# Kernel optimization log

Measured on AMD Instinct MI355X. Metric: run time of the kernel, lower is better.

## Reference

```python
import jax, jax.numpy as jnp
import numpy as np

N_NODES = 20000
N_EDGES = 640000
HIDDEN = 128


def setup_inputs() -> dict:
    key = jax.random.key(0)
    k1, k2, k3, k4 = jax.random.split(key, 4)
    scale = 1.0 / np.sqrt(HIDDEN)
    features = jax.random.normal(k1, (N_NODES, HIDDEN), dtype=jnp.float32)
    edge_index = jax.random.randint(k2, (2, N_EDGES), 0, N_NODES, dtype=jnp.int64)
    W_l = jax.random.normal(k3, (HIDDEN, HIDDEN), dtype=jnp.float32) * scale
    b_l = jnp.zeros((HIDDEN,), dtype=jnp.float32)
    W_r = jax.random.normal(k4, (HIDDEN, HIDDEN), dtype=jnp.float32) * scale
    return {"features": features, "edge_index": edge_index, "W_l": W_l, "b_l": b_l, "W_r": W_r}


def reference(features, edge_index, W_l, b_l, W_r):
    # PyG SAGEConv with mean aggregation:
    #   out_i = lin_l(mean_{j : (j->i) in E} x_j) + lin_r(x_i)
    # edge_index[0] = source nodes, edge_index[1] = target nodes.
    n = features.shape[0]
    src = edge_index[0]
    dst = edge_index[1]
    msg = features[src]  # [E, d] gather
    summed = jax.ops.segment_sum(msg, dst, num_segments=n)  # [N, d] scatter-add
    cnt = jax.ops.segment_sum(jnp.ones(src.shape[0], dtype=features.dtype), dst, num_segments=n)
    agg = summed / jnp.maximum(cnt, 1.0)[:, None]  # mean; isolated nodes -> 0
    return agg @ W_l.T + b_l + features @ W_r.T
```

## Files before the change

kernel.cpp:

```cpp
#include <hip/hip_runtime.h>

#define N_NODES 20000
#define N_EDGES 640000
#define HIDDEN  128
#define CAP     96
#define DEG_PAD 16
#define GEMM_BLOCKS 313
#define FILL_BLOCKS 2500

typedef unsigned short bf16_t;
typedef __attribute__((ext_vector_type(8))) short short8;
typedef __attribute__((ext_vector_type(4))) float floatx4;

__device__ __forceinline__ bf16_t f2bf(float f) {
    union { float f; unsigned int i; } v; v.f = f;
    unsigned int x = v.i + 0x7FFFu + ((v.i >> 16) & 1u);
    return (bf16_t)(x >> 16);
}
__device__ __forceinline__ float bflo(unsigned u) {
    union { unsigned i; float f; } v; v.i = u << 16; return v.f;
}
__device__ __forceinline__ float bfhi(unsigned u) {
    union { unsigned i; float f; } v; v.i = u & 0xFFFF0000u; return v.f;
}

__global__ void prep_kernel(const float* __restrict__ feat,
                            const float* __restrict__ Wl,
                            const float* __restrict__ Wr,
                            bf16_t* __restrict__ feat_bf,
                            bf16_t* __restrict__ Bp,
                            int* __restrict__ deg) {
    int t = blockIdx.x * 256 + threadIdx.x;
    float4 v = ((const float4*)feat)[t];
    ushort4 o = { f2bf(v.x), f2bf(v.y), f2bf(v.z), f2bf(v.w) };
    ((ushort4*)feat_bf)[t] = o;
    if (t < (N_NODES * DEG_PAD) / 4) {
        int4 zz = {0, 0, 0, 0};
        ((int4*)deg)[t] = zz;
    }
    if (t < 2 * HIDDEN * HIDDEN) {
        int j    = t & 7;
        int lane = (t >> 3) & 63;
        int nt   = (t >> 9) & 15;
        int kt   = t >> 13;
        int n = nt * 16 + (lane & 15);
        int k = kt * 32 + (lane >> 4) * 8 + j;
        float w = (n < HIDDEN) ? Wl[n * HIDDEN + k] : Wr[(n - HIDDEN) * HIDDEN + k];
        Bp[t] = f2bf(w);
    }
}

__global__ __launch_bounds__(256) void gemm_fill_kernel(
        const bf16_t* __restrict__ feat_bf,
        const bf16_t* __restrict__ Bp,
        const float* __restrict__ bl,
        const int* __restrict__ eidx,
        bf16_t* __restrict__ Y,
        float* __restrict__ Z,
        int* __restrict__ deg,
        int* __restrict__ bucket) {
    if (blockIdx.x < GEMM_BLOCKS) {
        int wid = blockIdx.x * 4 + (threadIdx.x >> 6);
        if (wid >= N_NODES / 16) return;
        int lane = threadIdx.x & 63;
        int m    = lane & 15;
        int quad = lane >> 4;
        int row0 = wid * 16;

        floatx4 acc[16];
        floatx4 zf = {0.f, 0.f, 0.f, 0.f};
#pragma unroll
        for (int nt = 0; nt < 16; ++nt) acc[nt] = zf;

        const short8* bp = (const short8*)Bp;
#pragma unroll
        for (int kt = 0; kt < 4; ++kt) {
            short8 afrag = *(const short8*)(feat_bf + (size_t)(row0 + m) * HIDDEN
                                            + kt * 32 + quad * 8);
#pragma unroll
            for (int nt = 0; nt < 16; ++nt) {
                short8 bfrag = bp[(kt * 16 + nt) * 64 + lane];
                acc[nt] = __builtin_amdgcn_mfma_f32_16x16x32_bf16(afrag, bfrag, acc[nt], 0, 0, 0);
            }
        }
        int col = lane & 15;
#pragma unroll
        for (int nt = 0; nt < 8; ++nt) {
#pragma unroll
            for (int r = 0; r < 4; ++r) {
                int row = row0 + quad * 4 + r;
                Y[(size_t)row * HIDDEN + nt * 16 + col] = f2bf(acc[nt][r]);
            }
        }
#pragma unroll
        for (int nt = 8; nt < 16; ++nt) {
            float b = bl[(nt - 8) * 16 + col];
#pragma unroll
            for (int r = 0; r < 4; ++r) {
                int row = row0 + quad * 4 + r;
                Z[(size_t)row * HIDDEN + (nt - 8) * 16 + col] = acc[nt][r] + b;
            }
        }
    } else {
        int e = (blockIdx.x - GEMM_BLOCKS) * 256 + threadIdx.x;
        if (e >= N_EDGES) return;
        int src = eidx[e];
        int dst = eidx[N_EDGES + e];
        int pos = atomicAdd(&deg[dst * DEG_PAD], 1);
        if (pos < CAP) bucket[dst * CAP + pos] = src;
    }
}

__global__ __launch_bounds__(256) void gather_final_kernel(
        const bf16_t* __restrict__ Y,
        const float* __restrict__ Z,
        const int* __restrict__ deg,
        const int* __restrict__ bucket,
        float* __restrict__ out) {
    int wid  = (blockIdx.x * 256 + threadIdx.x) >> 6;
    int lane = threadIdx.x & 63;
    if (wid >= N_NODES) return;
    int d_true = deg[wid * DEG_PAD];
    int d = min(d_true, CAP);
    const int* row = bucket + wid * CAP;
    const unsigned* y = (const unsigned*)Y;
    float ax0=0,ay0=0, ax1=0,ay1=0, ax2=0,ay2=0, ax3=0,ay3=0;
    int i = 0;
    for (; i + 4 <= d; i += 4) {
        int4 s = *(const int4*)(row + i);
        unsigned u0 = y[s.x * 64 + lane];
        unsigned u1 = y[s.y * 64 + lane];
        unsigned u2 = y[s.z * 64 + lane];
        unsigned u3 = y[s.w * 64 + lane];
        ax0 += bflo(u0); ay0 += bfhi(u0);
        ax1 += bflo(u1); ay1 += bfhi(u1);
        ax2 += bflo(u2); ay2 += bfhi(u2);
        ax3 += bflo(u3); ay3 += bfhi(u3);
    }
    for (; i < d; ++i) {
        unsigned u = y[row[i] * 64 + lane];
        ax0 += bflo(u); ay0 += bfhi(u);
    }
    float inv = 1.0f / fmaxf((float)d_true, 1.0f);
    float2 z = ((const float2*)Z)[wid * 64 + lane];
    float2 r;
    r.x = (ax0 + ax1 + ax2 + ax3) * inv + z.x;
    r.y = (ay0 + ay1 + ay2 + ay3) * inv + z.y;
    ((float2*)out)[wid * 64 + lane] = r;
}

extern "C" void kernel_launch(void* const* d_in, const int* in_sizes, int n_in,
                              void* d_out, int out_size, void* d_ws, size_t ws_size,
                              hipStream_t stream) {
    const float* feat = (const float*)d_in[0];
    const int*   eidx = (const int*)d_in[1];
    const float* Wl   = (const float*)d_in[2];
    const float* bl   = (const float*)d_in[3];
    const float* Wr   = (const float*)d_in[4];
    float* out = (float*)d_out;

    int*    deg     = (int*)d_ws;
    int*    bucket  = deg + N_NODES * DEG_PAD;
    bf16_t* Bp      = (bf16_t*)(bucket + N_NODES * CAP);
    bf16_t* feat_bf = Bp + 2 * HIDDEN * HIDDEN;
    bf16_t* Y       = feat_bf + (size_t)N_NODES * HIDDEN;
    float*  Z       = (float*)(Y + (size_t)N_NODES * HIDDEN);

    prep_kernel<<<2500, 256, 0, stream>>>(feat, Wl, Wr, feat_bf, Bp, deg);
    gemm_fill_kernel<<<GEMM_BLOCKS + FILL_BLOCKS, 256, 0, stream>>>(
        feat_bf, Bp, bl, eidx, Y, Z, deg, bucket);
    gather_final_kernel<<<(N_NODES * 64 + 255) / 256, 256, 0, stream>>>(
        Y, Z, deg, bucket, out);
}
```

Baseline: 142.1 us.

## Move edge bucketing into prep kernel, use 16-bit bucket indices, unroll gather by 8

The edge bucket fill now runs in the bf16 conversion kernel (each thread converts features and inserts one edge), and the degree array is zeroed with a memset. The GEMM gets its own kernel. Bucket entries shrink to 16-bit source indices, which halves bucket traffic, and the gather loop loads eight neighbours per iteration. This adds a memset launch and relies on node indices fitting in 16 bits, which holds since N_NODES is 20000.

```diff
diff --git a/kernel.cpp b/kernel.cpp
--- a/kernel.cpp
+++ b/kernel.cpp
@@ -5,11 +5,10 @@
 #define HIDDEN  128
 #define CAP     96
 #define DEG_PAD 16
-#define GEMM_BLOCKS 313
-#define FILL_BLOCKS 2500
 
 typedef unsigned short bf16_t;
 typedef __attribute__((ext_vector_type(8))) short short8;
+typedef __attribute__((ext_vector_type(8))) unsigned short ushort8_t;
 typedef __attribute__((ext_vector_type(4))) float floatx4;
 
 __device__ __forceinline__ bf16_t f2bf(float f) {
@@ -24,20 +23,23 @@
     union { unsigned i; float f; } v; v.i = u & 0xFFFF0000u; return v.f;
 }
 
-__global__ void prep_kernel(const float* __restrict__ feat,
-                            const float* __restrict__ Wl,
-                            const float* __restrict__ Wr,
-                            bf16_t* __restrict__ feat_bf,
-                            bf16_t* __restrict__ Bp,
-                            int* __restrict__ deg) {
+__global__ __launch_bounds__(256) void prep_fill_kernel(
+        const float* __restrict__ feat,
+        const float* __restrict__ Wl,
+        const float* __restrict__ Wr,
+        const int* __restrict__ eidx,
+        bf16_t* __restrict__ feat_bf,
+        bf16_t* __restrict__ Bp,
+        int* __restrict__ deg,
+        unsigned short* __restrict__ bucket) {
     int t = blockIdx.x * 256 + threadIdx.x;
     float4 v = ((const float4*)feat)[t];
     ushort4 o = { f2bf(v.x), f2bf(v.y), f2bf(v.z), f2bf(v.w) };
     ((ushort4*)feat_bf)[t] = o;
-    if (t < (N_NODES * DEG_PAD) / 4) {
-        int4 zz = {0, 0, 0, 0};
-        ((int4*)deg)[t] = zz;
-    }
+    int src = eidx[t];
+    int dst = eidx[N_EDGES + t];
+    int pos = atomicAdd(&deg[dst * DEG_PAD], 1);
+    if (pos < CAP) bucket[dst * CAP + pos] = (unsigned short)src;
     if (t < 2 * HIDDEN * HIDDEN) {
         int j    = t & 7;
         int lane = (t >> 3) & 63;
@@ -50,64 +52,52 @@
     }
 }
 
-__global__ __launch_bounds__(256) void gemm_fill_kernel(
+__global__ __launch_bounds__(256) void gemm_kernel(
         const bf16_t* __restrict__ feat_bf,
         const bf16_t* __restrict__ Bp,
         const float* __restrict__ bl,
-        const int* __restrict__ eidx,
         bf16_t* __restrict__ Y,
-        float* __restrict__ Z,
-        int* __restrict__ deg,
-        int* __restrict__ bucket) {
-    if (blockIdx.x < GEMM_BLOCKS) {
-        int wid = blockIdx.x * 4 + (threadIdx.x >> 6);
-        if (wid >= N_NODES / 16) return;
-        int lane = threadIdx.x & 63;
-        int m    = lane & 15;
-        int quad = lane >> 4;
-        int row0 = wid * 16;
+        float* __restrict__ Z) {
+    int wid = blockIdx.x * 4 + (threadIdx.x >> 6);
+    if (wid >= N_NODES / 16) return;
+    int lane = threadIdx.x & 63;
+    int m    = lane & 15;
+    int quad = lane >> 4;
+    int row0 = wid * 16;
 
-        floatx4 acc[16];
-        floatx4 zf = {0.f, 0.f, 0.f, 0.f};
+    floatx4 acc[16];
+    floatx4 zf = {0.f, 0.f, 0.f, 0.f};
 #pragma unroll
-        for (int nt = 0; nt < 16; ++nt) acc[nt] = zf;
+    for (int nt = 0; nt < 16; ++nt) acc[nt] = zf;
 
-        const short8* bp = (const short8*)Bp;
+    const short8* bp = (const short8*)Bp;
 #pragma unroll
-        for (int kt = 0; kt < 4; ++kt) {
-            short8 afrag = *(const short8*)(feat_bf + (size_t)(row0 + m) * HIDDEN
-                                            + kt * 32 + quad * 8);
+    for (int kt = 0; kt < 4; ++kt) {
+        short8 afrag = *(const short8*)(feat_bf + (size_t)(row0 + m) * HIDDEN
+                                        + kt * 32 + quad * 8);
 #pragma unroll
-            for (int nt = 0; nt < 16; ++nt) {
-                short8 bfrag = bp[(kt * 16 + nt) * 64 + lane];
-                acc[nt] = __builtin_amdgcn_mfma_f32_16x16x32_bf16(afrag, bfrag, acc[nt], 0, 0, 0);
-            }
+        for (int nt = 0; nt < 16; ++nt) {
+            short8 bfrag = bp[(kt * 16 + nt) * 64 + lane];
+            acc[nt] = __builtin_amdgcn_mfma_f32_16x16x32_bf16(afrag, bfrag, acc[nt], 0, 0, 0);
         }
-        int col = lane & 15;
+    }
+    int col = lane & 15;
 #pragma unroll
-        for (int nt = 0; nt < 8; ++nt) {
+    for (int nt = 0; nt < 8; ++nt) {
 #pragma unroll
-            for (int r = 0; r < 4; ++r) {
-                int row = row0 + quad * 4 + r;
-                Y[(size_t)row * HIDDEN + nt * 16 + col] = f2bf(acc[nt][r]);
-            }
+        for (int r = 0; r < 4; ++r) {
+            int row = row0 + quad * 4 + r;
+            Y[(size_t)row * HIDDEN + nt * 16 + col] = f2bf(acc[nt][r]);
         }
+    }
 #pragma unroll
-        for (int nt = 8; nt < 16; ++nt) {
-            float b = bl[(nt - 8) * 16 + col];
+    for (int nt = 8; nt < 16; ++nt) {
+        float b = bl[(nt - 8) * 16 + col];
 #pragma unroll
-            for (int r = 0; r < 4; ++r) {
-                int row = row0 + quad * 4 + r;
-                Z[(size_t)row * HIDDEN + (nt - 8) * 16 + col] = acc[nt][r] + b;
-            }
+        for (int r = 0; r < 4; ++r) {
+            int row = row0 + quad * 4 + r;
+            Z[(size_t)row * HIDDEN + (nt - 8) * 16 + col] = acc[nt][r] + b;
         }
-    } else {
-        int e = (blockIdx.x - GEMM_BLOCKS) * 256 + threadIdx.x;
-        if (e >= N_EDGES) return;
-        int src = eidx[e];
-        int dst = eidx[N_EDGES + e];
-        int pos = atomicAdd(&deg[dst * DEG_PAD], 1);
-        if (pos < CAP) bucket[dst * CAP + pos] = src;
     }
 }
 
@@ -115,30 +105,38 @@
         const bf16_t* __restrict__ Y,
         const float* __restrict__ Z,
         const int* __restrict__ deg,
-        const int* __restrict__ bucket,
+        const unsigned short* __restrict__ bucket,
         float* __restrict__ out) {
     int wid  = (blockIdx.x * 256 + threadIdx.x) >> 6;
     int lane = threadIdx.x & 63;
     if (wid >= N_NODES) return;
     int d_true = deg[wid * DEG_PAD];
     int d = min(d_true, CAP);
-    const int* row = bucket + wid * CAP;
+    const unsigned short* row = bucket + wid * CAP;
     const unsigned* y = (const unsigned*)Y;
     float ax0=0,ay0=0, ax1=0,ay1=0, ax2=0,ay2=0, ax3=0,ay3=0;
     int i = 0;
-    for (; i + 4 <= d; i += 4) {
-        int4 s = *(const int4*)(row + i);
-        unsigned u0 = y[s.x * 64 + lane];
-        unsigned u1 = y[s.y * 64 + lane];
-        unsigned u2 = y[s.z * 64 + lane];
-        unsigned u3 = y[s.w * 64 + lane];
+    for (; i + 8 <= d; i += 8) {
+        ushort8_t s = *(const ushort8_t*)(row + i);
+        unsigned u0 = y[(int)s[0] * 64 + lane];
+        unsigned u1 = y[(int)s[1] * 64 + lane];
+        unsigned u2 = y[(int)s[2] * 64 + lane];
+        unsigned u3 = y[(int)s[3] * 64 + lane];
+        unsigned u4 = y[(int)s[4] * 64 + lane];
+        unsigned u5 = y[(int)s[5] * 64 + lane];
+        unsigned u6 = y[(int)s[6] * 64 + lane];
+        unsigned u7 = y[(int)s[7] * 64 + lane];
         ax0 += bflo(u0); ay0 += bfhi(u0);
         ax1 += bflo(u1); ay1 += bfhi(u1);
         ax2 += bflo(u2); ay2 += bfhi(u2);
         ax3 += bflo(u3); ay3 += bfhi(u3);
+        ax0 += bflo(u4); ay0 += bfhi(u4);
+        ax1 += bflo(u5); ay1 += bfhi(u5);
+        ax2 += bflo(u6); ay2 += bfhi(u6);
+        ax3 += bflo(u7); ay3 += bfhi(u7);
     }
     for (; i < d; ++i) {
-        unsigned u = y[row[i] * 64 + lane];
+        unsigned u = y[(int)row[i] * 64 + lane];
         ax0 += bflo(u); ay0 += bfhi(u);
     }
     float inv = 1.0f / fmaxf((float)d_true, 1.0f);
@@ -159,16 +157,17 @@
     const float* Wr   = (const float*)d_in[4];
     float* out = (float*)d_out;
 
-    int*    deg     = (int*)d_ws;
-    int*    bucket  = deg + N_NODES * DEG_PAD;
-    bf16_t* Bp      = (bf16_t*)(bucket + N_NODES * CAP);
-    bf16_t* feat_bf = Bp + 2 * HIDDEN * HIDDEN;
-    bf16_t* Y       = feat_bf + (size_t)N_NODES * HIDDEN;
-    float*  Z       = (float*)(Y + (size_t)N_NODES * HIDDEN);
+    int*            deg     = (int*)d_ws;
+    unsigned short* bucket  = (unsigned short*)(deg + N_NODES * DEG_PAD);
+    bf16_t*         Bp      = (bf16_t*)(bucket + (size_t)N_NODES * CAP);
+    bf16_t*         feat_bf = Bp + 2 * HIDDEN * HIDDEN;
+    bf16_t*         Y       = feat_bf + (size_t)N_NODES * HIDDEN;
+    float*          Z       = (float*)(Y + (size_t)N_NODES * HIDDEN);
 
-    prep_kernel<<<2500, 256, 0, stream>>>(feat, Wl, Wr, feat_bf, Bp, deg);
-    gemm_fill_kernel<<<GEMM_BLOCKS + FILL_BLOCKS, 256, 0, stream>>>(
-        feat_bf, Bp, bl, eidx, Y, Z, deg, bucket);
-    gather_final_kernel<<<(N_NODES * 64 + 255) / 256, 256, 0, stream>>>(
-        Y, Z, deg, bucket, out);
+    hipMemsetAsync(deg, 0, (size_t)N_NODES * DEG_PAD * sizeof(int), stream);
+
+    prep_fill_kernel<<<N_EDGES / 256, 256, 0, stream>>>(
+        feat, Wl, Wr, eidx, feat_bf, Bp, deg, bucket);
+    gemm_kernel<<<(N_NODES / 16 + 3) / 4, 256, 0, stream>>>(feat_bf, Bp, bl, Y, Z);
+    gather_final_kernel<<<(N_NODES * 64) / 256, 256, 0, stream>>>(Y, Z, deg, bucket, out);
 }
```

Measured after the change: 136.3 us. -4.1%, faster.
